# Performance work log

Measured on AMD Instinct MI355X. Metric: run time of the kernel, lower is better.

Reference implementation:

```python
import jax, jax.numpy as jnp
import numpy as np

N, E, D_IN, D_OUT = 50000, 800000, 128, 128
EPS = 1e-5


def setup_inputs() -> dict:
    key = jax.random.key(0)
    ks = jax.random.split(key, 6)
    x = jax.random.normal(ks[0], (N, D_IN), dtype=jnp.float32)
    edge_index = jax.random.randint(ks[1], (2, E), 0, N, dtype=jnp.int64)
    # dropout mask with keep-prob 0.5, inverted-dropout scaling
    dropout_mask = (jax.random.uniform(ks[2], (N, D_IN)) > 0.5).astype(jnp.float32) * 2.0
    ln_weight = jnp.ones((D_IN,), jnp.float32)
    ln_bias = jnp.zeros((D_IN,), jnp.float32)
    w_l = jax.random.normal(ks[3], (D_IN, D_OUT), jnp.float32) / np.float32(np.sqrt(D_IN))
    b_l = jnp.zeros((D_OUT,), jnp.float32)
    w_r = jax.random.normal(ks[4], (D_IN, D_OUT), jnp.float32) / np.float32(np.sqrt(D_IN))
    return dict(x=x, edge_index=edge_index, dropout_mask=dropout_mask,
                ln_weight=ln_weight, ln_bias=ln_bias, w_l=w_l, b_l=b_l, w_r=w_r)


def reference(x, edge_index, dropout_mask, ln_weight, ln_bias, w_l, b_l, w_r):
    # PyG graph-mode LayerNorm (batch=None): normalize over all nodes & channels
    xc = x - jnp.mean(x)
    h = xc / (jnp.std(xc) + EPS) * ln_weight + ln_bias
    h = jax.nn.relu(h) * dropout_mask  # training path with dropout mask
    # SAGEConv (mean aggregation): aggregate source features into destinations
    src, dst = edge_index[0], edge_index[1]
    msg = h[src]  # [E, D_IN] gather
    agg = jax.ops.segment_sum(msg, dst, num_segments=N)  # [N, D_IN] scatter-add
    deg = jax.ops.segment_sum(jnp.ones((E,), h.dtype), dst, num_segments=N)
    agg = agg / jnp.maximum(deg, 1.0)[:, None]
    # out = lin_l(mean_aggr) + lin_r(x_root)
    return agg @ w_l + b_l + h @ w_r
```

## Files before the change

kernel.cpp:

```cpp
#include <hip/hip_runtime.h>
#include <math.h>

#define N_NODES 50000
#define N_EDGES 800000
#define D 128
#define EPS 1e-5f

#define WS_STATS_OFF   0
#define WS_CUR_OFF     16
#define WS_DEG_OFF     64
#define WS_OFFS_OFF    200192
#define WS_BUCKET_OFF  400448
#define WS_AGG_OFF     3600640
#define WS_H_OFF       29200896
#define WS_ZERO_BYTES  200192

#define RED_BLOCKS 1024
#define DEG_BLOCKS ((N_EDGES + 255) / 256)
#define H_BLOCKS   2048
#define FILL_BLOCKS DEG_BLOCKS

__global__ __launch_bounds__(256) void k_pre(const float* __restrict__ x,
                                             const int* __restrict__ ei,
                                             double* __restrict__ stats,
                                             int* __restrict__ deg,
                                             int total4) {
    __shared__ float bs[4], bss[4];
    if (blockIdx.x < RED_BLOCKS) {
        int tid = blockIdx.x * 256 + threadIdx.x;
        int stride = RED_BLOCKS * 256;
        float s = 0.f, ss = 0.f;
        for (int i = tid; i < total4; i += stride) {
            float4 v = ((const float4*)x)[i];
            s  += v.x + v.y + v.z + v.w;
            ss += v.x*v.x + v.y*v.y + v.z*v.z + v.w*v.w;
        }
        for (int off = 32; off; off >>= 1) {
            s  += __shfl_down(s, off);
            ss += __shfl_down(ss, off);
        }
        int lane = threadIdx.x & 63, wid = threadIdx.x >> 6;
        if (lane == 0) { bs[wid] = s; bss[wid] = ss; }
        __syncthreads();
        if (threadIdx.x == 0) {
            float t = 0.f, tt = 0.f;
            for (int w = 0; w < 4; ++w) { t += bs[w]; tt += bss[w]; }
            atomicAdd(stats, (double)t);
            atomicAdd(stats + 1, (double)tt);
        }
    } else {
        int e = (blockIdx.x - RED_BLOCKS) * 256 + threadIdx.x;
        if (e < N_EDGES) atomicAdd(deg + ei[N_EDGES + e], 1);
    }
}

__global__ __launch_bounds__(256) void k_offs(const int* __restrict__ deg,
                                              int* __restrict__ offs,
                                              int* __restrict__ cursor) {
    __shared__ int sc[256];
    __shared__ int sbase;
    int t = threadIdx.x;
    int n = blockIdx.x * 256 + t;
    int d = (n < N_NODES) ? deg[n] : 0;
    sc[t] = d;
    __syncthreads();
    for (int off = 1; off < 256; off <<= 1) {
        int u = (t >= off) ? sc[t - off] : 0;
        __syncthreads();
        sc[t] += u;
        __syncthreads();
    }
    int incl = sc[t];
    if (t == 255) sbase = atomicAdd(cursor, incl);
    __syncthreads();
    if (n < N_NODES) offs[n] = sbase + (incl - d);
}

__global__ __launch_bounds__(256) void k_hfill(const float* __restrict__ x,
                                               const float* __restrict__ mask,
                                               const float* __restrict__ lnw,
                                               const float* __restrict__ lnb,
                                               const double* __restrict__ stats,
                                               const int* __restrict__ ei,
                                               int* __restrict__ offs,
                                               int* __restrict__ bucket,
                                               float* __restrict__ h,
                                               int total4) {
    if (blockIdx.x < H_BLOCKS) {
        double M = (double)N_NODES * (double)D;
        double mean_d = stats[0] / M;
        double var = stats[1] / M - mean_d * mean_d;
        if (var < 0.0) var = 0.0;
        float mean = (float)mean_d;
        float rstd = (float)(1.0 / (sqrt(var) + (double)EPS));
        int tid = blockIdx.x * 256 + threadIdx.x;
        int stride = H_BLOCKS * 256;
        for (int i = tid; i < total4; i += stride) {
            float4 v = ((const float4*)x)[i];
            float4 m = ((const float4*)mask)[i];
            int c4 = i & (D / 4 - 1);
            float4 w = ((const float4*)lnw)[c4];
            float4 b = ((const float4*)lnb)[c4];
            float4 r;
            r.x = fmaxf((v.x - mean) * rstd * w.x + b.x, 0.f) * m.x;
            r.y = fmaxf((v.y - mean) * rstd * w.y + b.y, 0.f) * m.y;
            r.z = fmaxf((v.z - mean) * rstd * w.z + b.z, 0.f) * m.z;
            r.w = fmaxf((v.w - mean) * rstd * w.w + b.w, 0.f) * m.w;
            ((float4*)h)[i] = r;
        }
    } else {
        int e = (blockIdx.x - H_BLOCKS) * 256 + threadIdx.x;
        if (e < N_EDGES) {
            int dst = ei[N_EDGES + e];
            int p = atomicAdd(offs + dst, 1);
            bucket[p] = ei[e];
        }
    }
}

__global__ __launch_bounds__(256) void k_agg(const int* __restrict__ bucket,
                                             const int* __restrict__ offs,
                                             const int* __restrict__ deg,
                                             const float* __restrict__ h,
                                             float* __restrict__ agg) {
    int t = blockIdx.x * blockDim.x + threadIdx.x;
    int node = t >> 5;
    if (node >= N_NODES) return;
    int c = t & 31;
    int dg = deg[node];
    int end = offs[node];
    int start = end - dg;
    float4 acc = {0.f, 0.f, 0.f, 0.f};
    for (int j = start; j < end; ++j) {
        int src = bucket[j];
        float4 v = *(const float4*)(h + (long long)src * D + c * 4);
        acc.x += v.x; acc.y += v.y; acc.z += v.z; acc.w += v.w;
    }
    float inv = 1.0f / fmaxf((float)dg, 1.0f);
    float4 o = {acc.x * inv, acc.y * inv, acc.z * inv, acc.w * inv};
    *(float4*)(agg + (long long)node * D + c * 4) = o;
}

#define FMA4(A, S, W) { A.x += (S)*(W).x; A.y += (S)*(W).y; A.z += (S)*(W).z; A.w += (S)*(W).w; }

__global__ __launch_bounds__(256, 4) void k_mmf(const float* __restrict__ agg,
                                                const float* __restrict__ h,
                                                const float* __restrict__ w_l,
                                                const float* __restrict__ w_r,
                                                const float* __restrict__ b_l,
                                                float* __restrict__ out) {
    __shared__ float sw[64 * D];
    float4* sw4 = (float4*)sw;
    int ch4 = threadIdx.x & 31;
    int g   = threadIdx.x >> 5;
    int n0  = blockIdx.x * 64 + g * 8;
    int n0c = (n0 <= N_NODES - 8) ? n0 : (N_NODES - 8);

    float4 acc[8];
#pragma unroll
    for (int j = 0; j < 8; ++j) acc[j] = {0.f, 0.f, 0.f, 0.f};

#pragma unroll
    for (int phase = 0; phase < 2; ++phase) {
        const float4* wsrc4 = (const float4*)(phase == 0 ? w_l : w_r);
        const float4* rp4   = (const float4*)((phase == 0 ? agg : h) + (long long)n0c * D);
#pragma unroll
        for (int chunk = 0; chunk < 2; ++chunk) {
            if (phase | chunk) __syncthreads();
#pragma unroll
            for (int i = 0; i < 8; ++i)
                sw4[i * 256 + threadIdx.x] = wsrc4[chunk * 2048 + i * 256 + threadIdx.x];
            __syncthreads();

            for (int k0 = 0; k0 < 16; ++k0) {
                float4 r[8];
#pragma unroll
                for (int j = 0; j < 8; ++j)
                    r[j] = rp4[(j << 5) + chunk * 16 + k0];
#pragma unroll
                for (int kk = 0; kk < 4; ++kk) {
                    float4 wv = sw4[(k0 * 4 + kk) * 32 + ch4];
#pragma unroll
                    for (int j = 0; j < 8; ++j) {
                        float rj[4] = {r[j].x, r[j].y, r[j].z, r[j].w};
                        FMA4(acc[j], rj[kk], wv);
                    }
                }
            }
        }
    }

    float4 bl = ((const float4*)b_l)[ch4];
#pragma unroll
    for (int j = 0; j < 8; ++j) {
        int n = n0 + j;
        if (n < N_NODES) {
            float4 o = {acc[j].x + bl.x, acc[j].y + bl.y, acc[j].z + bl.z, acc[j].w + bl.w};
            *(float4*)(out + (long long)n * D + ch4 * 4) = o;
        }
    }
}

extern "C" void kernel_launch(void* const* d_in, const int* in_sizes, int n_in,
                              void* d_out, int out_size, void* d_ws, size_t ws_size,
                              hipStream_t stream) {
    const float* x    = (const float*)d_in[0];
    const int*   ei   = (const int*)d_in[1];
    const float* mask = (const float*)d_in[2];
    const float* lnw  = (const float*)d_in[3];
    const float* lnb  = (const float*)d_in[4];
    const float* w_l  = (const float*)d_in[5];
    const float* b_l  = (const float*)d_in[6];
    const float* w_r  = (const float*)d_in[7];
    float* out = (float*)d_out;

    char* ws = (char*)d_ws;
    double* stats = (double*)(ws + WS_STATS_OFF);
    int*    cursor= (int*)(ws + WS_CUR_OFF);
    int*    deg   = (int*)(ws + WS_DEG_OFF);
    int*    offs  = (int*)(ws + WS_OFFS_OFF);
    int*    bucket= (int*)(ws + WS_BUCKET_OFF);
    float*  agg   = (float*)(ws + WS_AGG_OFF);
    float*  h     = (float*)(ws + WS_H_OFF);

    hipMemsetAsync(d_ws, 0, WS_ZERO_BYTES, stream);

    int total4 = N_NODES * D / 4;
    k_pre<<<RED_BLOCKS + DEG_BLOCKS, 256, 0, stream>>>(x, ei, stats, deg, total4);
    k_offs<<<(N_NODES + 255) / 256, 256, 0, stream>>>(deg, offs, cursor);
    k_hfill<<<H_BLOCKS + FILL_BLOCKS, 256, 0, stream>>>(x, mask, lnw, lnb, stats,
                                                        ei, offs, bucket, h, total4);
    int ablocks = (N_NODES * 32 + 255) / 256;
    k_agg<<<ablocks, 256, 0, stream>>>(bucket, offs, deg, h, agg);
    int mblocks = (N_NODES + 63) / 64;
    k_mmf<<<mblocks, 256, 0, stream>>>(agg, h, w_l, w_r, b_l, out);
}
```

Measured before the change: 345.9 us.

## Store normalized features as bf16 and split matmul output channels across blocks

The normalized activation h is now stored as bf16 instead of fp32. This halves the bytes moved by the random gather in aggregation and by the root-term read in the fused matmul. The matmul kernel is also restructured into 128-thread blocks, each covering half the output channels, so each block needs only 32KB of shared memory for weights. The bf16 rounding of h adds numerical error to both the aggregated and root terms, and splitting channels means each block reads its input rows twice.

```diff
diff --git a/kernel.cpp b/kernel.cpp
--- a/kernel.cpp
+++ b/kernel.cpp
@@ -19,6 +19,11 @@
 #define DEG_BLOCKS ((N_EDGES + 255) / 256)
 #define H_BLOCKS   2048
 #define FILL_BLOCKS DEG_BLOCKS
+
+static __device__ inline unsigned short f2bf(float f) {
+    unsigned u = __float_as_uint(f);
+    return (unsigned short)((u + 0x7FFFu + ((u >> 16) & 1u)) >> 16);
+}
 
 __global__ __launch_bounds__(256) void k_pre(const float* __restrict__ x,
                                              const int* __restrict__ ei,
@@ -84,7 +89,7 @@
                                                const int* __restrict__ ei,
                                                int* __restrict__ offs,
                                                int* __restrict__ bucket,
-                                               float* __restrict__ h,
+                                               unsigned short* __restrict__ h16,
                                                int total4) {
     if (blockIdx.x < H_BLOCKS) {
         double M = (double)N_NODES * (double)D;
@@ -106,7 +111,9 @@
             r.y = fmaxf((v.y - mean) * rstd * w.y + b.y, 0.f) * m.y;
             r.z = fmaxf((v.z - mean) * rstd * w.z + b.z, 0.f) * m.z;
             r.w = fmaxf((v.w - mean) * rstd * w.w + b.w, 0.f) * m.w;
-            ((float4*)h)[i] = r;
+            ushort4 o;
+            o.x = f2bf(r.x); o.y = f2bf(r.y); o.z = f2bf(r.z); o.w = f2bf(r.w);
+            ((ushort4*)h16)[i] = o;
         }
     } else {
         int e = (blockIdx.x - H_BLOCKS) * 256 + threadIdx.x;
@@ -121,7 +128,7 @@
 __global__ __launch_bounds__(256) void k_agg(const int* __restrict__ bucket,
                                              const int* __restrict__ offs,
                                              const int* __restrict__ deg,
-                                             const float* __restrict__ h,
+                                             const unsigned short* __restrict__ h16,
                                              float* __restrict__ agg) {
     int t = blockIdx.x * blockDim.x + threadIdx.x;
     int node = t >> 5;
@@ -133,8 +140,11 @@
     float4 acc = {0.f, 0.f, 0.f, 0.f};
     for (int j = start; j < end; ++j) {
         int src = bucket[j];
-        float4 v = *(const float4*)(h + (long long)src * D + c * 4);
-        acc.x += v.x; acc.y += v.y; acc.z += v.z; acc.w += v.w;
+        uint2 u = *(const uint2*)(h16 + (long long)src * D + c * 4);
+        acc.x += __uint_as_float(u.x << 16);
+        acc.y += __uint_as_float(u.x & 0xFFFF0000u);
+        acc.z += __uint_as_float(u.y << 16);
+        acc.w += __uint_as_float(u.y & 0xFFFF0000u);
     }
     float inv = 1.0f / fmaxf((float)dg, 1.0f);
     float4 o = {acc.x * inv, acc.y * inv, acc.z * inv, acc.w * inv};
@@ -143,17 +153,19 @@
 
 #define FMA4(A, S, W) { A.x += (S)*(W).x; A.y += (S)*(W).y; A.z += (S)*(W).z; A.w += (S)*(W).w; }
 
-__global__ __launch_bounds__(256, 4) void k_mmf(const float* __restrict__ agg,
-                                                const float* __restrict__ h,
-                                                const float* __restrict__ w_l,
-                                                const float* __restrict__ w_r,
-                                                const float* __restrict__ b_l,
-                                                float* __restrict__ out) {
-    __shared__ float sw[64 * D];
-    float4* sw4 = (float4*)sw;
-    int ch4 = threadIdx.x & 31;
-    int g   = threadIdx.x >> 5;
-    int n0  = blockIdx.x * 64 + g * 8;
+__global__ __launch_bounds__(128) void k_mmf(const float* __restrict__ agg,
+                                             const unsigned short* __restrict__ h16,
+                                             const float* __restrict__ w_l,
+                                             const float* __restrict__ w_r,
+                                             const float* __restrict__ b_l,
+                                             float* __restrict__ out) {
+    __shared__ float4 sw4[64 * 16];
+    int tid = threadIdx.x;
+    int ch4 = tid & 15;
+    int g   = tid >> 4;
+    int tile  = blockIdx.x >> 1;
+    int chalf = blockIdx.x & 1;
+    int n0 = tile * 64 + g * 8;
     int n0c = (n0 <= N_NODES - 8) ? n0 : (N_NODES - 8);
 
     float4 acc[8];
@@ -163,40 +175,66 @@
 #pragma unroll
     for (int phase = 0; phase < 2; ++phase) {
         const float4* wsrc4 = (const float4*)(phase == 0 ? w_l : w_r);
-        const float4* rp4   = (const float4*)((phase == 0 ? agg : h) + (long long)n0c * D);
-#pragma unroll
-        for (int chunk = 0; chunk < 2; ++chunk) {
-            if (phase | chunk) __syncthreads();
-#pragma unroll
-            for (int i = 0; i < 8; ++i)
-                sw4[i * 256 + threadIdx.x] = wsrc4[chunk * 2048 + i * 256 + threadIdx.x];
+#pragma unroll
+        for (int ck = 0; ck < 2; ++ck) {
+            if (phase | ck) __syncthreads();
+#pragma unroll
+            for (int i = 0; i < 8; ++i) {
+                int f4 = i * 128 + tid;
+                int r = f4 >> 4, c4 = f4 & 15;
+                sw4[f4] = wsrc4[(ck * 64 + r) * 32 + chalf * 16 + c4];
+            }
             __syncthreads();
 
-            for (int k0 = 0; k0 < 16; ++k0) {
-                float4 r[8];
-#pragma unroll
-                for (int j = 0; j < 8; ++j)
-                    r[j] = rp4[(j << 5) + chunk * 16 + k0];
-#pragma unroll
-                for (int kk = 0; kk < 4; ++kk) {
-                    float4 wv = sw4[(k0 * 4 + kk) * 32 + ch4];
+            if (phase == 0) {
+                const float4* rp4 = (const float4*)(agg + (long long)n0c * D);
+                for (int k0 = 0; k0 < 16; ++k0) {
+                    float4 r[8];
+#pragma unroll
+                    for (int j = 0; j < 8; ++j) r[j] = rp4[j * 32 + ck * 16 + k0];
+#pragma unroll
+                    for (int kk = 0; kk < 4; ++kk) {
+                        float4 wv = sw4[(k0 * 4 + kk) * 16 + ch4];
+#pragma unroll
+                        for (int j = 0; j < 8; ++j) {
+                            float rj[4] = {r[j].x, r[j].y, r[j].z, r[j].w};
+                            FMA4(acc[j], rj[kk], wv);
+                        }
+                    }
+                }
+            } else {
+                const unsigned short* hp = h16 + (long long)n0c * D + ck * 64;
+                for (int k0 = 0; k0 < 16; ++k0) {
+                    float4 r[8];
 #pragma unroll
                     for (int j = 0; j < 8; ++j) {
-                        float rj[4] = {r[j].x, r[j].y, r[j].z, r[j].w};
-                        FMA4(acc[j], rj[kk], wv);
+                        uint2 u = *(const uint2*)(hp + j * D + k0 * 4);
+                        r[j].x = __uint_as_float(u.x << 16);
+                        r[j].y = __uint_as_float(u.x & 0xFFFF0000u);
+                        r[j].z = __uint_as_float(u.y << 16);
+                        r[j].w = __uint_as_float(u.y & 0xFFFF0000u);
+                    }
+#pragma unroll
+                    for (int kk = 0; kk < 4; ++kk) {
+                        float4 wv = sw4[(k0 * 4 + kk) * 16 + ch4];
+#pragma unroll
+                        for (int j = 0; j < 8; ++j) {
+                            float rj[4] = {r[j].x, r[j].y, r[j].z, r[j].w};
+                            FMA4(acc[j], rj[kk], wv);
+                        }
                     }
                 }
             }
         }
     }
 
-    float4 bl = ((const float4*)b_l)[ch4];
+    float4 bl = ((const float4*)b_l)[chalf * 16 + ch4];
 #pragma unroll
     for (int j = 0; j < 8; ++j) {
         int n = n0 + j;
         if (n < N_NODES) {
             float4 o = {acc[j].x + bl.x, acc[j].y + bl.y, acc[j].z + bl.z, acc[j].w + bl.w};
-            *(float4*)(out + (long long)n * D + ch4 * 4) = o;
+            *(float4*)(out + (long long)n * D + chalf * 64 + ch4 * 4) = o;
         }
     }
 }
@@ -221,7 +259,7 @@
     int*    offs  = (int*)(ws + WS_OFFS_OFF);
     int*    bucket= (int*)(ws + WS_BUCKET_OFF);
     float*  agg   = (float*)(ws + WS_AGG_OFF);
-    float*  h     = (float*)(ws + WS_H_OFF);
+    unsigned short* h16 = (unsigned short*)(ws + WS_H_OFF);
 
     hipMemsetAsync(d_ws, 0, WS_ZERO_BYTES, stream);
 
@@ -229,9 +267,9 @@
     k_pre<<<RED_BLOCKS + DEG_BLOCKS, 256, 0, stream>>>(x, ei, stats, deg, total4);
     k_offs<<<(N_NODES + 255) / 256, 256, 0, stream>>>(deg, offs, cursor);
     k_hfill<<<H_BLOCKS + FILL_BLOCKS, 256, 0, stream>>>(x, mask, lnw, lnb, stats,
-                                                        ei, offs, bucket, h, total4);
+                                                        ei, offs, bucket, h16, total4);
     int ablocks = (N_NODES * 32 + 255) / 256;
-    k_agg<<<ablocks, 256, 0, stream>>>(bucket, offs, deg, h, agg);
-    int mblocks = (N_NODES + 63) / 64;
-    k_mmf<<<mblocks, 256, 0, stream>>>(agg, h, w_l, w_r, b_l, out);
-}
+    k_agg<<<ablocks, 256, 0, stream>>>(bucket, offs, deg, h16, agg);
+    int mblocks = ((N_NODES + 63) / 64) * 2;
+    k_mmf<<<mblocks, 128, 0, stream>>>(agg, h16, w_l, w_r, b_l, out);
+}
```

Measured after the change: 340.5 us. Within noise of the previous version (-1.6%).

## Store h and agg in bf16 and use MFMA bf16 matmul with split weights

Applied to the files above, without the earlier changes.

Converts the normalized features h and the aggregated means to bf16, which halves the bytes moved by the random-gather aggregation and by the matmul reads. The fp32 FMA matmul is replaced with MFMA 16x16x32 bf16 instructions. The weights are pre-split by a new small kernel into hi and lo bf16 parts and stored transposed, so weight precision is kept. Activations are now rounded to bf16, which loosens accuracy against the fp32 reference.

```diff
diff --git a/kernel.cpp b/kernel.cpp
--- a/kernel.cpp
+++ b/kernel.cpp
@@ -11,14 +11,26 @@
 #define WS_DEG_OFF     64
 #define WS_OFFS_OFF    200192
 #define WS_BUCKET_OFF  400448
-#define WS_AGG_OFF     3600640
-#define WS_H_OFF       29200896
+#define WS_W16T_OFF    3600448
+#define WS_AGG_OFF     3731520
+#define WS_H_OFF       16531520
 #define WS_ZERO_BYTES  200192
 
 #define RED_BLOCKS 1024
 #define DEG_BLOCKS ((N_EDGES + 255) / 256)
 #define H_BLOCKS   2048
 #define FILL_BLOCKS DEG_BLOCKS
+
+typedef __attribute__((ext_vector_type(8))) short short8v;
+typedef __attribute__((ext_vector_type(4))) float f32x4;
+
+static __device__ inline unsigned short f2bf(float f) {
+    unsigned u = __float_as_uint(f);
+    return (unsigned short)((u + 0x7FFFu + ((u >> 16) & 1u)) >> 16);
+}
+static __device__ inline float bf2f(unsigned short s) {
+    return __uint_as_float(((unsigned)s) << 16);
+}
 
 __global__ __launch_bounds__(256) void k_pre(const float* __restrict__ x,
                                              const int* __restrict__ ei,
@@ -52,6 +64,27 @@
         int e = (blockIdx.x - RED_BLOCKS) * 256 + threadIdx.x;
         if (e < N_EDGES) atomicAdd(deg + ei[N_EDGES + e], 1);
     }
+}
+
+__global__ __launch_bounds__(256) void k_wprep(const float* __restrict__ w_l,
+                                               const float* __restrict__ w_r,
+                                               unsigned short* __restrict__ w16t) {
+    int t = blockIdx.x * 256 + threadIdx.x;
+    int p = t >> 12;
+    int o = (t >> 5) & 127;
+    int k4 = t & 31;
+    const float* w = p ? w_r : w_l;
+    ushort4 hi, lo;
+    float v0 = w[(k4 * 4 + 0) * D + o];
+    float v1 = w[(k4 * 4 + 1) * D + o];
+    float v2 = w[(k4 * 4 + 2) * D + o];
+    float v3 = w[(k4 * 4 + 3) * D + o];
+    hi.x = f2bf(v0); lo.x = f2bf(v0 - bf2f(hi.x));
+    hi.y = f2bf(v1); lo.y = f2bf(v1 - bf2f(hi.y));
+    hi.z = f2bf(v2); lo.z = f2bf(v2 - bf2f(hi.z));
+    hi.w = f2bf(v3); lo.w = f2bf(v3 - bf2f(hi.w));
+    *(ushort4*)(w16t + p * 32768 + o * D + k4 * 4) = hi;
+    *(ushort4*)(w16t + p * 32768 + 16384 + o * D + k4 * 4) = lo;
 }
 
 __global__ __launch_bounds__(256) void k_offs(const int* __restrict__ deg,
@@ -84,7 +117,7 @@
                                                const int* __restrict__ ei,
                                                int* __restrict__ offs,
                                                int* __restrict__ bucket,
-                                               float* __restrict__ h,
+                                               unsigned short* __restrict__ h16,
                                                int total4) {
     if (blockIdx.x < H_BLOCKS) {
         double M = (double)N_NODES * (double)D;
@@ -106,7 +139,9 @@
             r.y = fmaxf((v.y - mean) * rstd * w.y + b.y, 0.f) * m.y;
             r.z = fmaxf((v.z - mean) * rstd * w.z + b.z, 0.f) * m.z;
             r.w = fmaxf((v.w - mean) * rstd * w.w + b.w, 0.f) * m.w;
-            ((float4*)h)[i] = r;
+            ushort4 o;
+            o.x = f2bf(r.x); o.y = f2bf(r.y); o.z = f2bf(r.z); o.w = f2bf(r.w);
+            ((ushort4*)h16)[i] = o;
         }
     } else {
         int e = (blockIdx.x - H_BLOCKS) * 256 + threadIdx.x;
@@ -121,8 +156,8 @@
 __global__ __launch_bounds__(256) void k_agg(const int* __restrict__ bucket,
                                              const int* __restrict__ offs,
                                              const int* __restrict__ deg,
-                                             const float* __restrict__ h,
-                                             float* __restrict__ agg) {
+                                             const unsigned short* __restrict__ h16,
+                                             unsigned short* __restrict__ agg16) {
     int t = blockIdx.x * blockDim.x + threadIdx.x;
     int node = t >> 5;
     if (node >= N_NODES) return;
@@ -133,72 +168,57 @@
     float4 acc = {0.f, 0.f, 0.f, 0.f};
     for (int j = start; j < end; ++j) {
         int src = bucket[j];
-        float4 v = *(const float4*)(h + (long long)src * D + c * 4);
-        acc.x += v.x; acc.y += v.y; acc.z += v.z; acc.w += v.w;
+        uint2 u = *(const uint2*)(h16 + (long long)src * D + c * 4);
+        acc.x += __uint_as_float(u.x << 16);
+        acc.y += __uint_as_float(u.x & 0xFFFF0000u);
+        acc.z += __uint_as_float(u.y << 16);
+        acc.w += __uint_as_float(u.y & 0xFFFF0000u);
     }
     float inv = 1.0f / fmaxf((float)dg, 1.0f);
-    float4 o = {acc.x * inv, acc.y * inv, acc.z * inv, acc.w * inv};
-    *(float4*)(agg + (long long)node * D + c * 4) = o;
-}
-
-#define FMA4(A, S, W) { A.x += (S)*(W).x; A.y += (S)*(W).y; A.z += (S)*(W).z; A.w += (S)*(W).w; }
-
-__global__ __launch_bounds__(256, 4) void k_mmf(const float* __restrict__ agg,
-                                                const float* __restrict__ h,
-                                                const float* __restrict__ w_l,
-                                                const float* __restrict__ w_r,
-                                                const float* __restrict__ b_l,
-                                                float* __restrict__ out) {
-    __shared__ float sw[64 * D];
-    float4* sw4 = (float4*)sw;
-    int ch4 = threadIdx.x & 31;
-    int g   = threadIdx.x >> 5;
-    int n0  = blockIdx.x * 64 + g * 8;
-    int n0c = (n0 <= N_NODES - 8) ? n0 : (N_NODES - 8);
-
-    float4 acc[8];
+    ushort4 o;
+    o.x = f2bf(acc.x * inv); o.y = f2bf(acc.y * inv);
+    o.z = f2bf(acc.z * inv); o.w = f2bf(acc.w * inv);
+    *(ushort4*)(agg16 + (long long)node * D + c * 4) = o;
+}
+
+__global__ __launch_bounds__(256) void k_mmf(const unsigned short* __restrict__ agg16,
+                                             const unsigned short* __restrict__ h16,
+                                             const unsigned short* __restrict__ w16t,
+                                             const float* __restrict__ b_l,
+                                             float* __restrict__ out) {
+    int wid = (blockIdx.x << 2) | (threadIdx.x >> 6);
+    int lane = threadIdx.x & 63;
+    int nt = wid >> 3;
+    int ot = wid & 7;
+    int rc = lane & 15;
+    int kg = lane >> 4;
+
+    const unsigned short* pa = agg16 + ((long long)(nt * 16 + rc)) * D + kg * 8;
+    const unsigned short* ph = h16   + ((long long)(nt * 16 + rc)) * D + kg * 8;
+    const unsigned short* bl_hi = w16t + (ot * 16 + rc) * D + kg * 8;
+    const unsigned short* bl_lo = bl_hi + 16384;
+    const unsigned short* br_hi = bl_hi + 32768;
+    const unsigned short* br_lo = bl_hi + 49152;
+
+    f32x4 acc = {0.f, 0.f, 0.f, 0.f};
 #pragma unroll
-    for (int j = 0; j < 8; ++j) acc[j] = {0.f, 0.f, 0.f, 0.f};
-
+    for (int k0 = 0; k0 < 4; ++k0) {
+        short8v a = *(const short8v*)(pa + k0 * 32);
+        acc = __builtin_amdgcn_mfma_f32_16x16x32_bf16(a, *(const short8v*)(bl_hi + k0 * 32), acc, 0, 0, 0);
+        acc = __builtin_amdgcn_mfma_f32_16x16x32_bf16(a, *(const short8v*)(bl_lo + k0 * 32), acc, 0, 0, 0);
+    }
 #pragma unroll
-    for (int phase = 0; phase < 2; ++phase) {
-        const float4* wsrc4 = (const float4*)(phase == 0 ? w_l : w_r);
-        const float4* rp4   = (const float4*)((phase == 0 ? agg : h) + (long long)n0c * D);
+    for (int k0 = 0; k0 < 4; ++k0) {
+        short8v a = *(const short8v*)(ph + k0 * 32);
+        acc = __builtin_amdgcn_mfma_f32_16x16x32_bf16(a, *(const short8v*)(br_hi + k0 * 32), acc, 0, 0, 0);
+        acc = __builtin_amdgcn_mfma_f32_16x16x32_bf16(a, *(const short8v*)(br_lo + k0 * 32), acc, 0, 0, 0);
+    }
+
+    float bias = b_l[ot * 16 + rc];
+    float* op = out + ((long long)(nt * 16 + kg * 4)) * D + ot * 16 + rc;
 #pragma unroll
-        for (int chunk = 0; chunk < 2; ++chunk) {
-            if (phase | chunk) __syncthreads();
-#pragma unroll
-            for (int i = 0; i < 8; ++i)
-                sw4[i * 256 + threadIdx.x] = wsrc4[chunk * 2048 + i * 256 + threadIdx.x];
-            __syncthreads();
-
-            for (int k0 = 0; k0 < 16; ++k0) {
-                float4 r[8];
-#pragma unroll
-                for (int j = 0; j < 8; ++j)
-                    r[j] = rp4[(j << 5) + chunk * 16 + k0];
-#pragma unroll
-                for (int kk = 0; kk < 4; ++kk) {
-                    float4 wv = sw4[(k0 * 4 + kk) * 32 + ch4];
-#pragma unroll
-                    for (int j = 0; j < 8; ++j) {
-                        float rj[4] = {r[j].x, r[j].y, r[j].z, r[j].w};
-                        FMA4(acc[j], rj[kk], wv);
-                    }
-                }
-            }
-        }
-    }
-
-    float4 bl = ((const float4*)b_l)[ch4];
-#pragma unroll
-    for (int j = 0; j < 8; ++j) {
-        int n = n0 + j;
-        if (n < N_NODES) {
-            float4 o = {acc[j].x + bl.x, acc[j].y + bl.y, acc[j].z + bl.z, acc[j].w + bl.w};
-            *(float4*)(out + (long long)n * D + ch4 * 4) = o;
-        }
-    }
+    for (int r = 0; r < 4; ++r)
+        op[(long long)r * D] = acc[r] + bias;
 }
 
 extern "C" void kernel_launch(void* const* d_in, const int* in_sizes, int n_in,
@@ -220,18 +240,20 @@
     int*    deg   = (int*)(ws + WS_DEG_OFF);
     int*    offs  = (int*)(ws + WS_OFFS_OFF);
     int*    bucket= (int*)(ws + WS_BUCKET_OFF);
-    float*  agg   = (float*)(ws + WS_AGG_OFF);
-    float*  h     = (float*)(ws + WS_H_OFF);
+    unsigned short* w16t  = (unsigned short*)(ws + WS_W16T_OFF);
+    unsigned short* agg16 = (unsigned short*)(ws + WS_AGG_OFF);
+    unsigned short* h16   = (unsigned short*)(ws + WS_H_OFF);
 
     hipMemsetAsync(d_ws, 0, WS_ZERO_BYTES, stream);
 
     int total4 = N_NODES * D / 4;
     k_pre<<<RED_BLOCKS + DEG_BLOCKS, 256, 0, stream>>>(x, ei, stats, deg, total4);
+    k_wprep<<<32, 256, 0, stream>>>(w_l, w_r, w16t);
     k_offs<<<(N_NODES + 255) / 256, 256, 0, stream>>>(deg, offs, cursor);
     k_hfill<<<H_BLOCKS + FILL_BLOCKS, 256, 0, stream>>>(x, mask, lnw, lnb, stats,
-                                                        ei, offs, bucket, h, total4);
+                                                        ei, offs, bucket, h16, total4);
     int ablocks = (N_NODES * 32 + 255) / 256;
-    k_agg<<<ablocks, 256, 0, stream>>>(bucket, offs, deg, h, agg);
-    int mblocks = (N_NODES + 63) / 64;
-    k_mmf<<<mblocks, 256, 0, stream>>>(agg, h, w_l, w_r, b_l, out);
-}
+    k_agg<<<ablocks, 256, 0, stream>>>(bucket, offs, deg, h16, agg16);
+    int mblocks = (N_NODES / 16) * 8 / 4;
+    k_mmf<<<mblocks, 256, 0, stream>>>(agg16, h16, w16t, b_l, out);
+}
```

Measured after the change: 333.5 us. -3.6%, faster.
